# Kernel tuning notes

Hardware: AMD Instinct MI355X
Metric: run time of the kernel (lower is better)

Reference implementation:

```python
import jax, jax.numpy as jnp
import numpy as np

# dims: batch, seq, d_model, mlp_width, num_experts, lora_rank
B, S, D, M, E, R = 4, 1024, 2048, 5632, 8, 16
LORA_ALPHA = 32
SCALING = LORA_ALPHA / R  # = 2.0


def setup_inputs() -> dict:
    key = jax.random.key(0)
    ks = jax.random.split(key, 13)
    s = 0.02
    f32 = jnp.float32
    return {
        'x':  jax.random.normal(ks[0], (B, S, D), f32),
        # router: nn.Linear(d_model, num_experts)
        'Wr': jax.random.normal(ks[1], (E, D), f32) * s,
        'br': jax.random.normal(ks[2], (E,), f32) * s,
        # frozen original MLP weights (torch Linear layout [out, in])
        'Wg': jax.random.normal(ks[3], (M, D), f32) * s,
        'Wu': jax.random.normal(ks[4], (M, D), f32) * s,
        'Wd': jax.random.normal(ks[5], (D, M), f32) * s,
        # shared LoRA A matrices [rank, fan_in]
        'Ag': jax.random.normal(ks[6], (R, D), f32) * s,
        'Au': jax.random.normal(ks[7], (R, D), f32) * s,
        'Ad': jax.random.normal(ks[8], (R, M), f32) * s,
        # per-expert LoRA B matrices [E, fan_out, rank] (zero-init in the
        # original; randomized here so gradients/outputs are non-trivial)
        'Bg': jax.random.normal(ks[9], (E, M, R), f32) * s,
        'Bu': jax.random.normal(ks[10], (E, M, R), f32) * s,
        'Bd': jax.random.normal(ks[11], (E, D, R), f32) * s,
    }


def _lora_moe_dense(x, W, A, Bexp, routing):
    """Dense MoE LoRA: original_proj(x) + sum_e routing[...,e] * (x @ A^T @ B_e^T) * scaling.
    x: [b,s,in], W: [out,in], A: [r,in], Bexp: [E,out,r], routing: [b,s,E].
    Identical math to stacking all experts then weighted-summing, but the
    shared A lets us weight the tiny [b,s,E,r] hidden instead of [b,s,E,out].
    """
    orig = jnp.einsum('bsi,oi->bso', x, W)
    h = jnp.einsum('bsi,ri->bsr', x, A)            # shared low-rank hidden
    hw = jnp.einsum('bsr,bse->bser', h, routing)   # routing-weighted hidden
    lora = jnp.einsum('bser,eor->bso', hw, Bexp) * SCALING
    return orig + lora


def reference(x, Wr, br, Wg, Wu, Wd, Ag, Au, Ad, Bg, Bu, Bd):
    logits = jnp.einsum('bsd,ed->bse', x, Wr) + br
    routing = jax.nn.softmax(logits, axis=-1)
    idx = jnp.argmax(routing, axis=-1)
    y_hard = jax.nn.one_hot(idx, E, dtype=logits.dtype)
    # straight-through expert choice
    expert_choice = y_hard - jax.lax.stop_gradient(routing) + routing
    gate = _lora_moe_dense(x, Wg, Ag, Bg, routing)
    up = _lora_moe_dense(x, Wu, Au, Bu, routing)
    h = jax.nn.silu(gate) * up  # LLaMA-style SwiGLU act_fn
    out = _lora_moe_dense(h, Wd, Ad, Bd, routing)
    return out, routing, expert_choice
```

## Files before the change

### kernel.cpp

```cpp
#include <hip/hip_runtime.h>

#define DEV __device__ __forceinline__

typedef unsigned short u16;
typedef __bf16 bf16x8 __attribute__((ext_vector_type(8)));
typedef float f32x4 __attribute__((ext_vector_type(4)));

static DEV u16 f2bf(float f) {
    union { float f; unsigned u; } v; v.f = f;
    unsigned r = v.u + 0x7fffu + ((v.u >> 16) & 1u);
    return (u16)(r >> 16);
}
static DEV float bf2f(u16 u) {
    union { unsigned u; float f; } v; v.u = ((unsigned)u) << 16;
    return v.f;
}
static DEV void g2l16(const u16* g, u16* l) {
    __builtin_amdgcn_global_load_lds(
        (const __attribute__((address_space(1))) void*)g,
        (__attribute__((address_space(3))) void*)l, 16, 0, 0);
}

#define BAR()    do { __builtin_amdgcn_s_barrier(); __builtin_amdgcn_sched_barrier(0); } while (0)
#define WAITV(N) asm volatile("s_waitcnt vmcnt(" #N ")" ::: "memory")

#define MM16(A, B, FMO, FNO) do {                                            \
    __builtin_amdgcn_s_setprio(1);                                           \
    _Pragma("unroll")                                                        \
    for (int fm_ = 0; fm_ < 4; ++fm_)                                        \
      _Pragma("unroll")                                                      \
      for (int fn_ = 0; fn_ < 2; ++fn_)                                      \
        _Pragma("unroll")                                                    \
        for (int ks_ = 0; ks_ < 2; ++ks_)                                    \
          acc[(FMO) + fm_][(FNO) + fn_] = __builtin_amdgcn_mfma_f32_16x16x32_bf16( \
              A[fm_][ks_], B[fn_][ks_], acc[(FMO) + fm_][(FNO) + fn_], 0, 0, 0); \
    __builtin_amdgcn_s_setprio(0);                                           \
} while (0)


__global__ __launch_bounds__(256) void k_conv(
    const float* __restrict__ Wg, const float* __restrict__ Wu, const float* __restrict__ Wd,
    const float* __restrict__ Bg, const float* __restrict__ Bu, const float* __restrict__ Bd,
    u16* __restrict__ Wg16, u16* __restrict__ Wu16, u16* __restrict__ Wd16,
    u16* __restrict__ Bgx, u16* __restrict__ Bux, u16* __restrict__ Bdx)
{
    const long long NW = 2883584;
    const long long NB = 180224;
    const long long ND = 65536;
    long long gid = (long long)blockIdx.x * 256 + threadIdx.x;
    if (gid < 3 * NW) {
        const float* s; u16* d; long long g = gid;
        if (g < NW)           { s = Wg; d = Wg16; }
        else if (g < 2 * NW)  { s = Wu; d = Wu16; g -= NW; }
        else                  { s = Wd; d = Wd16; g -= 2 * NW; }
        float4 v = *(const float4*)(s + g * 4);
        ushort4 o; o.x = f2bf(v.x); o.y = f2bf(v.y); o.z = f2bf(v.z); o.w = f2bf(v.w);
        *(ushort4*)(d + g * 4) = o;
    } else {
        long long g = gid - 3 * NW;
        const float* s; u16* d; int nr;
        if (g < NB)               { s = Bg; d = Bgx; nr = 5632; }
        else if (g < 2 * NB)      { s = Bu; d = Bux; nr = 5632; g -= NB; }
        else if (g < 2 * NB + ND) { s = Bd; d = Bdx; nr = 2048; g -= 2 * NB; }
        else return;
        int n = (int)(g >> 5);
        int j0 = ((int)g & 31) * 4;
        int e = j0 >> 4, r0 = j0 & 15;
        float4 v = *(const float4*)&s[((size_t)e * nr + n) * 16 + r0];
        ushort4 o; o.x = f2bf(v.x); o.y = f2bf(v.y); o.z = f2bf(v.z); o.w = f2bf(v.w);
        *(ushort4*)&d[(size_t)n * 128 + j0] = o;
    }
}

__global__ __launch_bounds__(256) void k_router(
    const float* __restrict__ x, const float* __restrict__ Wr,
    const float* __restrict__ Ag, const float* __restrict__ Au,
    u16* __restrict__ x16, float* __restrict__ fin1)
{
    __shared__ float xs[64][65];
    __shared__ float wsm[40][64];
    const int rb = blockIdx.x, ksp = blockIdx.y;
    const int row0 = rb * 64;
    const int t = threadIdx.x;
    const int rloc = t & 63, og = t >> 6;
    float acc[10];
#pragma unroll
    for (int o = 0; o < 10; ++o) acc[o] = 0.f;

    for (int c4 = 0; c4 < 4; ++c4) {
        const int k0 = ksp * 256 + c4 * 64;
        __syncthreads();
#pragma unroll
        for (int i = 0; i < 4; ++i) {
            int idx = t + i * 256;
            int r = idx >> 4, c = (idx & 15) * 4;
            float4 v = *(const float4*)&x[(size_t)(row0 + r) * 2048 + k0 + c];
            xs[r][c + 0] = v.x; xs[r][c + 1] = v.y; xs[r][c + 2] = v.z; xs[r][c + 3] = v.w;
            ushort4 o; o.x = f2bf(v.x); o.y = f2bf(v.y); o.z = f2bf(v.z); o.w = f2bf(v.w);
            *(ushort4*)&x16[(size_t)(row0 + r) * 2048 + k0 + c] = o;
        }
#pragma unroll
        for (int i = 0; i < 3; ++i) {
            int idx = t + i * 256;
            if (idx < 640) {
                int r = idx >> 4, c = (idx & 15) * 4;
                const float* src = (r < 8) ? (Wr + (size_t)r * 2048)
                                : (r < 24) ? (Ag + (size_t)(r - 8) * 2048)
                                           : (Au + (size_t)(r - 24) * 2048);
                float4 v = *(const float4*)&src[k0 + c];
                wsm[r][c + 0] = v.x; wsm[r][c + 1] = v.y; wsm[r][c + 2] = v.z; wsm[r][c + 3] = v.w;
            }
        }
        __syncthreads();
#pragma unroll
        for (int k = 0; k < 64; ++k) {
            float xv = xs[rloc][k];
#pragma unroll
            for (int o = 0; o < 10; ++o) acc[o] += xv * wsm[og * 10 + o][k];
        }
    }
    float* dst = fin1 + ((size_t)ksp * 4096 + row0 + rloc) * 40 + og * 10;
#pragma unroll
    for (int o = 0; o < 10; ++o) dst[o] = acc[o];
}

__global__ __launch_bounds__(64) void k_fin1(
    const float* __restrict__ fin1, const float* __restrict__ br,
    float* __restrict__ routing_ws, float* __restrict__ out_rt, float* __restrict__ out_ec,
    u16* __restrict__ hwg, u16* __restrict__ hwu)
{
    const int row = blockIdx.x * 64 + threadIdx.x;
    float s[40];
#pragma unroll
    for (int j = 0; j < 40; ++j) s[j] = 0.f;
    for (int p = 0; p < 8; ++p) {
        const float* src = fin1 + ((size_t)p * 4096 + row) * 40;
#pragma unroll
        for (int j = 0; j < 40; ++j) s[j] += src[j];
    }
    float lg[8]; float m = -1e30f;
#pragma unroll
    for (int e = 0; e < 8; ++e) { lg[e] = s[e] + br[e]; m = fmaxf(m, lg[e]); }
    float ex[8]; float sum = 0.f;
#pragma unroll
    for (int e = 0; e < 8; ++e) { ex[e] = expf(lg[e] - m); sum += ex[e]; }
    float r8[8];
#pragma unroll
    for (int e = 0; e < 8; ++e) r8[e] = ex[e] / sum;
    int best = 0;
#pragma unroll
    for (int e = 1; e < 8; ++e) if (r8[e] > r8[best]) best = e;
#pragma unroll
    for (int e = 0; e < 8; ++e) {
        routing_ws[(size_t)row * 8 + e] = r8[e];
        out_rt[(size_t)row * 8 + e] = r8[e];
        float yh = (e == best) ? 1.f : 0.f;
        out_ec[(size_t)row * 8 + e] = (yh - r8[e]) + r8[e];
    }
#pragma unroll
    for (int e = 0; e < 8; ++e) {
        float re = r8[e];
#pragma unroll
        for (int rk = 0; rk < 16; ++rk) {
            hwg[(size_t)row * 128 + e * 16 + rk] = f2bf(2.f * s[8 + rk] * re);
            hwu[(size_t)row * 128 + e * 16 + rk] = f2bf(2.f * s[24 + rk] * re);
        }
    }
}

template<int MODE>
__global__ __launch_bounds__(512, 2) void k_gemm8(
    const u16* __restrict__ A0, int lda0,
    const u16* __restrict__ A1g, const u16* __restrict__ A1u,
    const u16* __restrict__ B0g, int ldb0, const u16* __restrict__ B0u,
    const u16* __restrict__ B1g, const u16* __restrict__ B1u,
    int Ksplit,
    float* __restrict__ outF0, float* __restrict__ outF1,
    u16* __restrict__ outHg, u16* __restrict__ outHu,
    int nbm, int nbn)
{
    __shared__ u16 lds[65536];
    const int t = threadIdx.x;
    const int nwg = (int)gridDim.x;
    const int orig = (int)blockIdx.x;
    const int sw = (orig & 7) * (nwg >> 3) + (orig >> 3);
    const int bm = sw % nbm; const int rest = sw / nbm;
    const int bn = rest % nbn; const int z = rest / nbn;

    const int row0 = bm * 256, col0 = bn * 256;
    int ktb, ntl;
    if (MODE == 0) { ktb = z ? 46 : 0; ntl = z ? 44 : 46; }
    else           { ktb = 0;          ntl = 34; }
    const int kend = ktb + ntl;
    const u16* A1 = (MODE == 1 && z) ? A1u : A1g;
    const u16* B0 = (MODE == 1 && z) ? B0u : B0g;
    const u16* B1 = (MODE == 1 && z) ? B1u : B1g;

    const int lane = t & 63, lr = lane & 15, lg = lane >> 4;
    const int wid = t >> 6, wr = wid >> 2, wcol = wid & 3;
    const int arow = wr * 128 + lr;
    const int brow = wcol * 64 + lr;
    const int sa = (arow & 7) << 3;
    const int sb = (brow & 7) << 3;

    const int rA = t >> 3;
    const int c00u = ((t & 7) * 8) ^ ((rA & 7) << 3);
    const u16* bA0 = A0 + (size_t)(row0 + rA) * lda0 + c00u;
    const u16* bA1 = A1 + ((size_t)(row0 + rA) << 7) + c00u;
    const u16* bB0 = B0 + (size_t)(col0 + rA) * ldb0 + c00u;
    const u16* bB1 = B1 + ((size_t)(col0 + rA) << 7) + c00u;
    const int ldsT = t * 8;

    auto stgA = [&](int kt, int h, int bufu) {
        const int k0 = kt * 64;
        const bool p2 = (k0 >= Ksplit);
        const u16* b = p2 ? (bA1 + (k0 - Ksplit)) : (bA0 + k0);
        const size_t ld = p2 ? (size_t)128 : (size_t)lda0;
        g2l16(b + (size_t)(h * 128) * ld,      &lds[bufu + h * 8192 + ldsT]);
        g2l16(b + (size_t)(h * 128 + 64) * ld, &lds[bufu + h * 8192 + 4096 + ldsT]);
    };
    auto stgB = [&](int kt, int h, int bufu) {
        const int k0 = kt * 64;
        const bool p2 = (k0 >= Ksplit);
        const u16* b = p2 ? (bB1 + (k0 - Ksplit)) : (bB0 + k0);
        const size_t ld = p2 ? (size_t)128 : (size_t)ldb0;
        g2l16(b + (size_t)(h * 128) * ld,      &lds[32768 + bufu + h * 8192 + ldsT]);
        g2l16(b + (size_t)(h * 128 + 64) * ld, &lds[32768 + bufu + h * 8192 + 4096 + ldsT]);
    };
    auto rdA = [&](int bufu, int fb, bf16x8 (&d)[4][2]) {
#pragma unroll
        for (int fm = 0; fm < 4; ++fm)
#pragma unroll
            for (int ks = 0; ks < 2; ++ks)
                d[fm][ks] = *(const bf16x8*)&lds[bufu + (arow + (fb + fm) * 16) * 64
                                                 + (((ks << 5) | (lg << 3)) ^ sa)];
    };
    auto rdB = [&](int bufu, int fb, bf16x8 (&d)[2][2]) {
#pragma unroll
        for (int fn = 0; fn < 2; ++fn)
#pragma unroll
            for (int ks = 0; ks < 2; ++ks)
                d[fn][ks] = *(const bf16x8*)&lds[32768 + bufu + (brow + (fb + fn) * 16) * 64
                                                 + (((ks << 5) | (lg << 3)) ^ sb)];
    };

    f32x4 acc[8][4];
    const f32x4 zf = {0.f, 0.f, 0.f, 0.f};
#pragma unroll
    for (int i = 0; i < 8; ++i)
#pragma unroll
        for (int j = 0; j < 4; ++j) acc[i][j] = zf;

    stgA(ktb, 0, 0); stgA(ktb, 1, 0);
    stgB(ktb, 0, 0); stgB(ktb, 1, 0);
    stgB(ktb + 1, 0, 16384); stgB(ktb + 1, 1, 16384);
    WAITV(4);
    BAR();

    const int ni = ntl >> 1;
    for (int i = 0; i < ni; ++i) {
        const int kt0 = ktb + 2 * i, kt1 = kt0 + 1;
        const bool s2 = (kt0 + 2 < kend), s3 = (kt1 + 2 < kend);
        bf16x8 alo[4][2], ahi[4][2], b01[2][2], b23[2][2];
        rdA(0, 0, alo); rdB(0, 0, b01); rdB(0, 2, b23);
        stgA(kt1, 0, 16384); stgA(kt1, 1, 16384);
        BAR();
        MM16(alo, b01, 0, 0); MM16(alo, b23, 0, 2);
        BAR();
        rdA(0, 4, ahi);
        if (s2) { stgB(kt0 + 2, 0, 0); stgB(kt0 + 2, 1, 0); }
        BAR();
        MM16(ahi, b01, 4, 0); MM16(ahi, b23, 4, 2);
        if (s2) { WAITV(4); } else { WAITV(0); }
        BAR();
        rdA(16384, 0, alo); rdB(16384, 0, b01); rdB(16384, 2, b23);
        if (s2) { stgA(kt0 + 2, 0, 0); stgA(kt0 + 2, 1, 0); }
        BAR();
        MM16(alo, b01, 0, 0); MM16(alo, b23, 0, 2);
        BAR();
        rdA(16384, 4, ahi);
        if (s3) { stgB(kt1 + 2, 0, 16384); stgB(kt1 + 2, 1, 16384); }
        BAR();
        MM16(ahi, b01, 4, 0); MM16(ahi, b23, 4, 2);
        if (s3) { WAITV(4); }
        BAR();
    }

#pragma unroll
    for (int fm = 0; fm < 8; ++fm) {
#pragma unroll
        for (int fn = 0; fn < 4; ++fn) {
            const int r = row0 + wr * 128 + fm * 16 + lg * 4;
            const int c = col0 + wcol * 64 + fn * 16 + lr;
            f32x4 v = acc[fm][fn];
            if constexpr (MODE == 0) {
                float* out = z ? outF1 : outF0;
#pragma unroll
                for (int j = 0; j < 4; ++j) out[(size_t)(r + j) * 2048 + c] = v[j];
            } else {
                u16* out = z ? outHu : outHg;
#pragma unroll
                for (int j = 0; j < 4; ++j) out[(size_t)(r + j) * 5632 + c] = f2bf(v[j]);
            }
        }
    }
}

__global__ __launch_bounds__(256) void k_hd(
    u16* __restrict__ g, const u16* __restrict__ u,
    const float* __restrict__ Ad, float* __restrict__ fin2)
{
    __shared__ float hs[64][65];
    __shared__ float as2[16][64];
    const int rb = blockIdx.x, ksp = blockIdx.y;
    const int row0 = rb * 64;
    const int t = threadIdx.x;
    const int rloc = t & 63, og = t >> 6;
    float acc[4] = {0.f, 0.f, 0.f, 0.f};
    for (int c4 = 0; c4 < 8; ++c4) {
        const int k0 = ksp * 512 + c4 * 64;
        __syncthreads();
#pragma unroll
        for (int i = 0; i < 4; ++i) {
            int idx = t + i * 256;
            int r = idx >> 4, cc = (idx & 15) * 4;
            size_t go = (size_t)(row0 + r) * 5632 + k0 + cc;
            ushort4 gv = *(const ushort4*)&g[go];
            ushort4 uv = *(const ushort4*)&u[go];
            float h0, h1, h2, h3;
            { float gg = bf2f(gv.x); h0 = gg / (1.f + __expf(-gg)) * bf2f(uv.x); }
            { float gg = bf2f(gv.y); h1 = gg / (1.f + __expf(-gg)) * bf2f(uv.y); }
            { float gg = bf2f(gv.z); h2 = gg / (1.f + __expf(-gg)) * bf2f(uv.z); }
            { float gg = bf2f(gv.w); h3 = gg / (1.f + __expf(-gg)) * bf2f(uv.w); }
            hs[r][cc + 0] = h0; hs[r][cc + 1] = h1; hs[r][cc + 2] = h2; hs[r][cc + 3] = h3;
            ushort4 hv; hv.x = f2bf(h0); hv.y = f2bf(h1); hv.z = f2bf(h2); hv.w = f2bf(h3);
            *(ushort4*)&g[go] = hv;
        }
        {
            int r = t >> 4, cc = (t & 15) * 4;
            float4 w = *(const float4*)&Ad[(size_t)r * 5632 + k0 + cc];
            as2[r][cc + 0] = w.x; as2[r][cc + 1] = w.y; as2[r][cc + 2] = w.z; as2[r][cc + 3] = w.w;
        }
        __syncthreads();
#pragma unroll
        for (int k = 0; k < 64; ++k) {
            float hv = hs[rloc][k];
#pragma unroll
            for (int o = 0; o < 4; ++o) acc[o] += hv * as2[og * 4 + o][k];
        }
    }
    float* dst = fin2 + ((size_t)ksp * 4096 + row0 + rloc) * 16 + og * 4;
#pragma unroll
    for (int o = 0; o < 4; ++o) dst[o] = acc[o];
}

__global__ __launch_bounds__(64) void k_fin2(
    const float* __restrict__ fin2, const float* __restrict__ routing_ws, u16* __restrict__ hwd)
{
    const int row = blockIdx.x * 64 + threadIdx.x;
    float hd[16];
#pragma unroll
    for (int j = 0; j < 16; ++j) hd[j] = 0.f;
    for (int p = 0; p < 11; ++p) {
        const float* src = fin2 + ((size_t)p * 4096 + row) * 16;
#pragma unroll
        for (int j = 0; j < 16; ++j) hd[j] += src[j];
    }
#pragma unroll
    for (int e = 0; e < 8; ++e) {
        float re = routing_ws[(size_t)row * 8 + e];
#pragma unroll
        for (int rk = 0; rk < 16; ++rk)
            hwd[(size_t)row * 128 + e * 16 + rk] = f2bf(2.f * hd[rk] * re);
    }
}

__global__ __launch_bounds__(256) void k_reduce(
    float* __restrict__ o, const float* __restrict__ p1)
{
    size_t i = ((size_t)blockIdx.x * 256 + threadIdx.x) * 4;
    float4 a = *(const float4*)&o[i];
    float4 b = *(const float4*)&p1[i];
    float4 r; r.x = a.x + b.x; r.y = a.y + b.y; r.z = a.z + b.z; r.w = a.w + b.w;
    *(float4*)&o[i] = r;
}

extern "C" void kernel_launch(void* const* d_in, const int* in_sizes, int n_in,
                              void* d_out, int out_size, void* d_ws, size_t ws_size,
                              hipStream_t stream)
{
    (void)in_sizes; (void)n_in; (void)out_size; (void)ws_size;
    const float* x  = (const float*)d_in[0];
    const float* Wr = (const float*)d_in[1];
    const float* br = (const float*)d_in[2];
    const float* Wg = (const float*)d_in[3];
    const float* Wu = (const float*)d_in[4];
    const float* Wd = (const float*)d_in[5];
    const float* Ag = (const float*)d_in[6];
    const float* Au = (const float*)d_in[7];
    const float* Ad = (const float*)d_in[8];
    const float* Bg = (const float*)d_in[9];
    const float* Bu = (const float*)d_in[10];
    const float* Bd = (const float*)d_in[11];

    float* outp   = (float*)d_out;
    float* out_rt = outp + 8388608;
    float* out_ec = out_rt + 32768;

    char* p = (char*)d_ws;
    auto carve = [&](size_t n) -> char* { char* r = p; p += (n + 255) & ~(size_t)255; return r; };
    u16*   x16        = (u16*)carve(16777216);
    u16*   hwg        = (u16*)carve(1048576);
    u16*   hwu        = (u16*)carve(1048576);
    u16*   hwd        = (u16*)carve(1048576);
    float* routing_ws = (float*)carve(131072);
    float* fin1       = (float*)carve(5242880);
    float* fin2       = (float*)carve(2883584);
    u16*   Wg16       = (u16*)carve(23068672);
    u16*   Wu16       = (u16*)carve(23068672);
    u16*   Wd16      = (u16*)carve(23068672);
    u16*   Bgx        = (u16*)carve(1441792);
    u16*   Bux        = (u16*)carve(1441792);
    u16*   Bdx        = (u16*)carve(524288);
    u16*   gbuf       = (u16*)carve(46137344);
    u16*   ubuf       = (u16*)carve(46137344);
    float* part1      = (float*)ubuf;

    k_conv<<<dim3(35456), dim3(256), 0, stream>>>(Wg, Wu, Wd, Bg, Bu, Bd,
                                                  Wg16, Wu16, Wd16, Bgx, Bux, Bdx);
    k_router<<<dim3(64, 8), dim3(256), 0, stream>>>(x, Wr, Ag, Au, x16, fin1);
    k_fin1<<<dim3(64), dim3(64), 0, stream>>>(fin1, br, routing_ws, out_rt, out_ec, hwg, hwu);
    k_gemm8<1><<<dim3(704), dim3(512), 0, stream>>>(
        x16, 2048, hwg, hwu, Wg16, 2048, Wu16, Bgx, Bux,
        2048, (float*)nullptr, (float*)nullptr, gbuf, ubuf, 16, 22);
    k_hd<<<dim3(64, 11), dim3(256), 0, stream>>>(gbuf, ubuf, Ad, fin2);
    k_fin2<<<dim3(64), dim3(64), 0, stream>>>(fin2, routing_ws, hwd);
    k_gemm8<0><<<dim3(256), dim3(512), 0, stream>>>(
        gbuf, 5632, hwd, hwd, Wd16, 5632, Wd16, Bdx, Bdx,
        5632, outp, part1, (u16*)nullptr, (u16*)nullptr, 16, 8);
    k_reduce<<<dim3(8192), dim3(256), 0, stream>>>(outp, part1);
}
```

Baseline: 431.8 us.

## Replace split-K partial buffer and reduce kernel with atomic adds into zeroed output

```diff
diff --git a/kernel.cpp b/kernel.cpp
--- a/kernel.cpp
+++ b/kernel.cpp
@@ -42,12 +42,20 @@
     const float* __restrict__ Wg, const float* __restrict__ Wu, const float* __restrict__ Wd,
     const float* __restrict__ Bg, const float* __restrict__ Bu, const float* __restrict__ Bd,
     u16* __restrict__ Wg16, u16* __restrict__ Wu16, u16* __restrict__ Wd16,
-    u16* __restrict__ Bgx, u16* __restrict__ Bux, u16* __restrict__ Bdx)
+    u16* __restrict__ Bgx, u16* __restrict__ Bux, u16* __restrict__ Bdx,
+    float* __restrict__ outp)
 {
     const long long NW = 2883584;
     const long long NB = 180224;
     const long long ND = 65536;
-    long long gid = (long long)blockIdx.x * 256 + threadIdx.x;
+    const int bid = blockIdx.x;
+    if (bid >= 35456) {
+        size_t i = ((size_t)(bid - 35456) * 256 + threadIdx.x) * 4;
+        float4 z; z.x = 0.f; z.y = 0.f; z.z = 0.f; z.w = 0.f;
+        *(float4*)&outp[i] = z;
+        return;
+    }
+    long long gid = (long long)bid * 256 + threadIdx.x;
     if (gid < 3 * NW) {
         const float* s; u16* d; long long g = gid;
         if (g < NW)           { s = Wg; d = Wg16; }
@@ -112,11 +120,19 @@
             }
         }
         __syncthreads();
-#pragma unroll
-        for (int k = 0; k < 64; ++k) {
-            float xv = xs[rloc][k];
-#pragma unroll
-            for (int o = 0; o < 10; ++o) acc[o] += xv * wsm[og * 10 + o][k];
+        float xr[64];
+#pragma unroll
+        for (int k = 0; k < 64; ++k) xr[k] = xs[rloc][k];
+#pragma unroll
+        for (int o = 0; o < 10; ++o) {
+#pragma unroll
+            for (int kk = 0; kk < 16; ++kk) {
+                float4 w4 = *(const float4*)&wsm[og * 10 + o][kk * 4];
+                acc[o] += xr[kk * 4 + 0] * w4.x;
+                acc[o] += xr[kk * 4 + 1] * w4.y;
+                acc[o] += xr[kk * 4 + 2] * w4.z;
+                acc[o] += xr[kk * 4 + 3] * w4.w;
+            }
         }
     }
     float* dst = fin1 + ((size_t)ksp * 4096 + row0 + rloc) * 40 + og * 10;
@@ -175,7 +191,7 @@
     const u16* __restrict__ B0g, int ldb0, const u16* __restrict__ B0u,
     const u16* __restrict__ B1g, const u16* __restrict__ B1u,
     int Ksplit,
-    float* __restrict__ outF0, float* __restrict__ outF1,
+    float* __restrict__ outF0,
     u16* __restrict__ outHg, u16* __restrict__ outHu,
     int nbm, int nbn)
 {
@@ -294,9 +310,9 @@
             const int c = col0 + wcol * 64 + fn * 16 + lr;
             f32x4 v = acc[fm][fn];
             if constexpr (MODE == 0) {
-                float* out = z ? outF1 : outF0;
-#pragma unroll
-                for (int j = 0; j < 4; ++j) out[(size_t)(r + j) * 2048 + c] = v[j];
+#pragma unroll
+                for (int j = 0; j < 4; ++j)
+                    atomicAdd(&outF0[(size_t)(r + j) * 2048 + c], v[j]);
             } else {
                 u16* out = z ? outHu : outHg;
 #pragma unroll
@@ -375,16 +391,6 @@
     }
 }
 
-__global__ __launch_bounds__(256) void k_reduce(
-    float* __restrict__ o, const float* __restrict__ p1)
-{
-    size_t i = ((size_t)blockIdx.x * 256 + threadIdx.x) * 4;
-    float4 a = *(const float4*)&o[i];
-    float4 b = *(const float4*)&p1[i];
-    float4 r; r.x = a.x + b.x; r.y = a.y + b.y; r.z = a.z + b.z; r.w = a.w + b.w;
-    *(float4*)&o[i] = r;
-}
-
 extern "C" void kernel_launch(void* const* d_in, const int* in_sizes, int n_in,
                               void* d_out, int out_size, void* d_ws, size_t ws_size,
                               hipStream_t stream)
@@ -418,25 +424,23 @@
     float* fin2       = (float*)carve(2883584);
     u16*   Wg16       = (u16*)carve(23068672);
     u16*   Wu16       = (u16*)carve(23068672);
-    u16*   Wd16      = (u16*)carve(23068672);
+    u16*   Wd16       = (u16*)carve(23068672);
     u16*   Bgx        = (u16*)carve(1441792);
     u16*   Bux        = (u16*)carve(1441792);
     u16*   Bdx        = (u16*)carve(524288);
     u16*   gbuf       = (u16*)carve(46137344);
     u16*   ubuf       = (u16*)carve(46137344);
-    float* part1      = (float*)ubuf;
-
-    k_conv<<<dim3(35456), dim3(256), 0, stream>>>(Wg, Wu, Wd, Bg, Bu, Bd,
-                                                  Wg16, Wu16, Wd16, Bgx, Bux, Bdx);
+
+    k_conv<<<dim3(43648), dim3(256), 0, stream>>>(Wg, Wu, Wd, Bg, Bu, Bd,
+                                                  Wg16, Wu16, Wd16, Bgx, Bux, Bdx, outp);
     k_router<<<dim3(64, 8), dim3(256), 0, stream>>>(x, Wr, Ag, Au, x16, fin1);
     k_fin1<<<dim3(64), dim3(64), 0, stream>>>(fin1, br, routing_ws, out_rt, out_ec, hwg, hwu);
     k_gemm8<1><<<dim3(704), dim3(512), 0, stream>>>(
         x16, 2048, hwg, hwu, Wg16, 2048, Wu16, Bgx, Bux,
-        2048, (float*)nullptr, (float*)nullptr, gbuf, ubuf, 16, 22);
+        2048, (float*)nullptr, gbuf, ubuf, 16, 22);
     k_hd<<<dim3(64, 11), dim3(256), 0, stream>>>(gbuf, ubuf, Ad, fin2);
     k_fin2<<<dim3(64), dim3(64), 0, stream>>>(fin2, routing_ws, hwd);
     k_gemm8<0><<<dim3(256), dim3(512), 0, stream>>>(
         gbuf, 5632, hwd, hwd, Wd16, 5632, Wd16, Bdx, Bdx,
-        5632, outp, part1, (u16*)nullptr, (u16*)nullptr, 16, 8);
-    k_reduce<<<dim3(8192), dim3(256), 0, stream>>>(outp, part1);
-}
+        5632, outp, (u16*)nullptr, (u16*)nullptr, 16, 8);
+}
```

After: 456.9 us. 5.8% more time.
